# Kernel tuning notes

Hardware: AMD Instinct MI355X
Metric: run time of the kernel (lower is better)

The kernel has to match this reference:

```python
import jax, jax.numpy as jnp
import numpy as np

POOL_H, POOL_W = 7, 7


def _crop_and_resize(fmap, boxes, box_idx, ph, pw):
    """TF tf.image.crop_and_resize (bilinear) for normalized boxes.
    fmap: [B,H,W,C], boxes: [M,4] (y1,x1,y2,x2), box_idx: [M] int32 -> [M,ph,pw,C]."""
    H, W = fmap.shape[1], fmap.shape[2]
    dt = fmap.dtype
    y1, x1, y2, x2 = jnp.split(boxes.astype(dt), 4, axis=1)  # each [M,1]
    gy = jnp.arange(ph, dtype=dt) / (ph - 1)
    gx = jnp.arange(pw, dtype=dt) / (pw - 1)
    ys = (y1 + (y2 - y1) * gy[None, :]) * (H - 1)  # [M,ph]
    xs = (x1 + (x2 - x1) * gx[None, :]) * (W - 1)  # [M,pw]
    y0 = jnp.clip(jnp.floor(ys), 0, H - 1).astype(jnp.int32)
    x0 = jnp.clip(jnp.floor(xs), 0, W - 1).astype(jnp.int32)
    y1i = jnp.minimum(y0 + 1, H - 1)
    x1i = jnp.minimum(x0 + 1, W - 1)
    ly = (ys - y0.astype(dt))[:, :, None, None]  # [M,ph,1,1]
    lx = (xs - x0.astype(dt))[:, None, :, None]  # [M,1,pw,1]
    b = box_idx[:, None, None]
    tl = fmap[b, y0[:, :, None], x0[:, None, :]]   # [M,ph,pw,C]
    tr = fmap[b, y0[:, :, None], x1i[:, None, :]]
    bl = fmap[b, y1i[:, :, None], x0[:, None, :]]
    br = fmap[b, y1i[:, :, None], x1i[:, None, :]]
    top = tl + (tr - tl) * lx
    bot = bl + (br - bl) * lx
    return top + (bot - top) * ly


def pyramid_roi_align(boxes, image_meta, feature_maps):
    B, N, _ = boxes.shape
    y1, x1, y2, x2 = jnp.split(boxes, 4, axis=2)
    h = y2 - y1
    w = x2 - x1
    image_shape = image_meta[0, 4:7]
    image_area = image_shape[0] * image_shape[1]
    roi_level = jnp.log2(jnp.sqrt(h * w) / (224.0 / jnp.sqrt(image_area)))
    roi_level = jnp.clip(4 + jnp.round(roi_level).astype(jnp.int32), 2, 5)
    roi_level = roi_level.reshape(B * N)  # squeeze axis 2 + flatten

    flat_boxes = boxes.reshape(B * N, 4)
    box_idx = jnp.repeat(jnp.arange(B, dtype=jnp.int32), N)
    C = feature_maps[0].shape[-1]
    pooled = jnp.zeros((B * N, POOL_H, POOL_W, C), dtype=feature_maps[0].dtype)
    # Equivalent to TF's gather/crop/sort-restore: each box pooled from its level.
    for i, level in enumerate(range(2, 6)):
        crop = _crop_and_resize(feature_maps[i], flat_boxes, box_idx, POOL_H, POOL_W)
        mask = (roi_level == level)[:, None, None, None]
        pooled = jnp.where(mask, crop, pooled)
    return pooled.reshape(B, N, POOL_H, POOL_W, C)


def setup_inputs() -> dict:
    key = jax.random.key(0)
    k1, k2, k3, k4, k5, k6, k7, k8 = jax.random.split(key, 8)
    B, N, C = 2, 1000, 256
    # boxes: normalized y1,x1,y2,x2 with sizes spanning all FPN levels
    sz = jax.random.uniform(k1, (B, N, 1), minval=0.02, maxval=0.8)
    yx1 = jax.random.uniform(k2, (B, N, 2)) * (1.0 - sz)
    boxes = jnp.concatenate([yx1[..., :1], yx1[..., 1:], yx1[..., :1] + sz, yx1[..., 1:] + sz], axis=2)
    # image_meta: image_shape (1024,1024,3) at indices 4:7
    meta = np.zeros((B, 93), dtype=np.float32)
    meta[:, 1:4] = [1024, 1024, 3]
    meta[:, 4:7] = [1024, 1024, 3]
    meta[:, 11] = 1.0
    return {
        "boxes": boxes.astype(jnp.float32),
        "image_meta": jnp.asarray(meta),
        "feat_p2": jax.random.normal(k3, (B, 256, 256, C), dtype=jnp.float32),
        "feat_p3": jax.random.normal(k4, (B, 128, 128, C), dtype=jnp.float32),
        "feat_p4": jax.random.normal(k5, (B, 64, 64, C), dtype=jnp.float32),
        "feat_p5": jax.random.normal(k6, (B, 32, 32, C), dtype=jnp.float32),
    }


def reference(boxes, image_meta, feat_p2, feat_p3, feat_p4, feat_p5):
    return pyramid_roi_align(boxes, image_meta, (feat_p2, feat_p3, feat_p4, feat_p5))
```

## Files before the change

### kernel.cpp

```cpp
#include <hip/hip_runtime.h>
#include <math.h>


#define POOLN 7
#define CCH 256

typedef float f32x4 __attribute__((ext_vector_type(4)));

struct __align__(16) PixRec {
    int   tl, tr, bl, br;
    float lx, ly;
    int   li, pad;
};

__global__ __launch_bounds__(256) void roi_prep_kernel(
    const float* __restrict__ boxes,
    const float* __restrict__ meta,
    PixRec* __restrict__ recs,
    int n_boxes, int boxes_per_batch)
{
    int t = blockIdx.x * blockDim.x + threadIdx.x;
    int total = n_boxes * 49;
    if (t >= total) return;

    int box = t / 49;
    int p   = t - box * 49;
    int py  = (p * 37) >> 8;
    int px  = p - py * 7;

    float by1 = boxes[4 * box + 0];
    float bx1 = boxes[4 * box + 1];
    float by2 = boxes[4 * box + 2];
    float bx2 = boxes[4 * box + 3];
    float h = by2 - by1, w = bx2 - bx1;

    float area  = meta[4] * meta[5];
    float scale = 224.0f / sqrtf(area);
    float rl    = log2f(sqrtf(h * w) / scale);
    int lvl = 4 + (int)rintf(rl);
    lvl = lvl < 2 ? 2 : (lvl > 5 ? 5 : lvl);
    int li = lvl - 2;
    int H  = 256 >> li;
    float hm1 = (float)(H - 1);
    int b = box / boxes_per_batch;

    float gy  = (float)py / 6.0f;
    float ys  = (by1 + h * gy) * hm1;
    float fy0 = fminf(fmaxf(floorf(ys), 0.0f), hm1);
    int y0  = (int)fy0;
    int y1i = min(y0 + 1, H - 1);

    float gx  = (float)px / 6.0f;
    float xs  = (bx1 + w * gx) * hm1;
    float fx0 = fminf(fmaxf(floorf(xs), 0.0f), hm1);
    int x0  = (int)fx0;
    int x1i = min(x0 + 1, H - 1);

    int row0 = (b * H + y0)  * H;
    int row1 = (b * H + y1i) * H;

    PixRec r;
    r.tl = (row0 + x0)  * CCH;
    r.tr = (row0 + x1i) * CCH;
    r.bl = (row1 + x0)  * CCH;
    r.br = (row1 + x1i) * CCH;
    r.lx = xs - fx0;
    r.ly = ys - fy0;
    r.li = li;
    r.pad = 0;
    recs[t] = r;
}

__device__ __forceinline__ f32x4 bilerp4(f32x4 tl, f32x4 tr, f32x4 bl, f32x4 br,
                                         float lx, float ly)
{
    f32x4 r;
    float top, bot;
    top = tl.x + (tr.x - tl.x) * lx; bot = bl.x + (br.x - bl.x) * lx; r.x = top + (bot - top) * ly;
    top = tl.y + (tr.y - tl.y) * lx; bot = bl.y + (br.y - bl.y) * lx; r.y = top + (bot - top) * ly;
    top = tl.z + (tr.z - tl.z) * lx; bot = bl.z + (br.z - bl.z) * lx; r.z = top + (bot - top) * ly;
    top = tl.w + (tr.w - tl.w) * lx; bot = bl.w + (br.w - bl.w) * lx; r.w = top + (bot - top) * ly;
    return r;
}

__global__ __launch_bounds__(256) void roi_gather_kernel(
    const PixRec* __restrict__ recs,
    const float* __restrict__ f2,
    const float* __restrict__ f3,
    const float* __restrict__ f4,
    const float* __restrict__ f5,
    float* __restrict__ out,
    int q, int r, long total)
{
    int bid    = blockIdx.x;
    int xcd    = bid & 7;
    int within = bid >> 3;
    int wg = (xcd < r ? xcd * (q + 1) : r * (q + 1) + (xcd - r) * q) + within;

    long wid = (long)wg * 256 + threadIdx.x;
    if (wid >= total) return;

    int  c4  = (int)(wid & 31);
    long t   = wid >> 5;

    PixRec rec = recs[t];
    const float* f = (rec.li == 0) ? f2 : (rec.li == 1) ? f3 : (rec.li == 2) ? f4 : f5;
    float lx = rec.lx, ly = rec.ly;

    int co = c4 * 4;
    const float* ptl = f + rec.tl + co;
    const float* ptr2= f + rec.tr + co;
    const float* pbl = f + rec.bl + co;
    const float* pbr = f + rec.br + co;

    f32x4 tlA = *(const f32x4*)ptl;
    f32x4 trA = *(const f32x4*)ptr2;
    f32x4 blA = *(const f32x4*)pbl;
    f32x4 brA = *(const f32x4*)pbr;
    f32x4 tlB = *(const f32x4*)(ptl + 128);
    f32x4 trB = *(const f32x4*)(ptr2 + 128);
    f32x4 blB = *(const f32x4*)(pbl + 128);
    f32x4 brB = *(const f32x4*)(pbr + 128);

    f32x4 rA = bilerp4(tlA, trA, blA, brA, lx, ly);
    f32x4 rB = bilerp4(tlB, trB, blB, brB, lx, ly);

    long obase = t * CCH + co;
    __builtin_nontemporal_store(rA, (f32x4*)(out + obase));
    __builtin_nontemporal_store(rB, (f32x4*)(out + obase + 128));
}

__global__ __launch_bounds__(256) void roi_align_kernel(
    const float* __restrict__ boxes,
    const float* __restrict__ meta,
    const float* __restrict__ f2,
    const float* __restrict__ f3,
    const float* __restrict__ f4,
    const float* __restrict__ f5,
    float* __restrict__ out,
    int boxes_per_batch,
    long total4)
{
    long idx = (long)blockIdx.x * blockDim.x + threadIdx.x;
    if (idx >= total4) return;

    int c4  = (int)(idx & 63);
    long t  = idx >> 6;
    int p   = (int)(t % 49);
    int box = (int)(t / 49);
    int py = p / 7, px = p % 7;

    float by1 = boxes[4 * box + 0];
    float bx1 = boxes[4 * box + 1];
    float by2 = boxes[4 * box + 2];
    float bx2 = boxes[4 * box + 3];

    float h = by2 - by1, w = bx2 - bx1;
    float area  = meta[4] * meta[5];
    float scale = 224.0f / sqrtf(area);
    float rl    = log2f(sqrtf(h * w) / scale);
    int lvl = 4 + (int)rintf(rl);
    lvl = lvl < 2 ? 2 : (lvl > 5 ? 5 : lvl);
    int li = lvl - 2;
    const float* f = (li == 0) ? f2 : (li == 1) ? f3 : (li == 2) ? f4 : f5;
    int H = 256 >> li;

    int b = box / boxes_per_batch;

    float gy = (float)py / 6.0f;
    float gx = (float)px / 6.0f;
    float ys = (by1 + (by2 - by1) * gy) * (float)(H - 1);
    float xs = (bx1 + (bx2 - bx1) * gx) * (float)(H - 1);

    float fy0 = fminf(fmaxf(floorf(ys), 0.0f), (float)(H - 1));
    float fx0 = fminf(fmaxf(floorf(xs), 0.0f), (float)(H - 1));
    int y0 = (int)fy0, x0 = (int)fx0;
    int y1i = min(y0 + 1, H - 1);
    int x1i = min(x0 + 1, H - 1);
    float ly = ys - fy0;
    float lx = xs - fx0;

    size_t row0 = ((size_t)b * H + y0)  * H;
    size_t row1 = ((size_t)b * H + y1i) * H;
    const f32x4* tl = (const f32x4*)(f + (row0 + x0)  * CCH) + c4;
    const f32x4* tr = (const f32x4*)(f + (row0 + x1i) * CCH) + c4;
    const f32x4* bl = (const f32x4*)(f + (row1 + x0)  * CCH) + c4;
    const f32x4* br = (const f32x4*)(f + (row1 + x1i) * CCH) + c4;

    f32x4 rr = bilerp4(*tl, *tr, *bl, *br, lx, ly);
    ((f32x4*)out)[idx] = rr;
}

extern "C" void kernel_launch(void* const* d_in, const int* in_sizes, int n_in,
                              void* d_out, int out_size, void* d_ws, size_t ws_size,
                              hipStream_t stream) {
    const float* boxes = (const float*)d_in[0];
    const float* meta  = (const float*)d_in[1];
    const float* f2    = (const float*)d_in[2];
    const float* f3    = (const float*)d_in[3];
    const float* f4    = (const float*)d_in[4];
    const float* f5    = (const float*)d_in[5];
    float* out         = (float*)d_out;

    int n_boxes = in_sizes[0] / 4;
    int B       = in_sizes[2] / (256 * 256 * 256);
    int boxes_per_batch = n_boxes / B;

    int    n_pix = n_boxes * 49;
    size_t need  = (size_t)n_pix * sizeof(PixRec);

    if (d_ws != nullptr && ws_size >= need) {
        PixRec* recs = (PixRec*)d_ws;

        roi_prep_kernel<<<(n_pix + 255) / 256, 256, 0, stream>>>(
            boxes, meta, recs, n_boxes, boxes_per_batch);

        long total = (long)n_pix * 32;
        int  nwg   = (int)((total + 255) / 256);
        int  q = nwg >> 3, r = nwg & 7;
        roi_gather_kernel<<<nwg, 256, 0, stream>>>(
            recs, f2, f3, f4, f5, out, q, r, total);
    } else {
        long total4 = (long)n_boxes * 49 * 64;
        int  blocks = (int)((total4 + 255) / 256);
        roi_align_kernel<<<blocks, 256, 0, stream>>>(
            boxes, meta, f2, f3, f4, f5, out, boxes_per_batch, total4);
    }
}
```

Before: 42.61 us.

## Process boxes grouped by pyramid level via counting-sort order in gather

Adds a single-block kernel that computes each box's FPN level and builds a level-sorted box order using a shared-memory counting sort. The gather kernel then visits boxes in that order, so consecutive workgroups read from the same feature map, which should improve cache locality. The XCD-aware block remapping is removed in the same change. The cost is an extra serial one-block launch and an indirection load per thread. Because atomic ranks are nondeterministic, the order within a level is not stable.

```diff
diff --git a/kernel.cpp b/kernel.cpp
--- a/kernel.cpp
+++ b/kernel.cpp
@@ -12,6 +12,45 @@
     float lx, ly;
     int   li, pad;
 };
+
+__global__ __launch_bounds__(1024) void roi_sort_kernel(
+    const float* __restrict__ boxes,
+    const float* __restrict__ meta,
+    int* __restrict__ order,
+    int* __restrict__ li_box,
+    int* __restrict__ rank_box,
+    int n_boxes)
+{
+    __shared__ int scnt[4];
+    __shared__ int sbase[4];
+    int tid = threadIdx.x;
+    if (tid < 4) scnt[tid] = 0;
+    __syncthreads();
+
+    float area  = meta[4] * meta[5];
+    float scale = 224.0f / sqrtf(area);
+
+    for (int b = tid; b < n_boxes; b += blockDim.x) {
+        float by1 = boxes[4*b+0], bx1 = boxes[4*b+1];
+        float by2 = boxes[4*b+2], bx2 = boxes[4*b+3];
+        float h = by2 - by1, w = bx2 - bx1;
+        float rl = log2f(sqrtf(h * w) / scale);
+        int lvl = 4 + (int)rintf(rl);
+        lvl = lvl < 2 ? 2 : (lvl > 5 ? 5 : lvl);
+        int li = lvl - 2;
+        li_box[b]   = li;
+        rank_box[b] = atomicAdd(&scnt[li], 1);
+    }
+    __syncthreads();
+    if (tid == 0) {
+        int acc = 0;
+        for (int i = 0; i < 4; ++i) { sbase[i] = acc; acc += scnt[i]; }
+    }
+    __syncthreads();
+    for (int b = tid; b < n_boxes; b += blockDim.x) {
+        order[sbase[li_box[b]] + rank_box[b]] = b;
+    }
+}
 
 __global__ __launch_bounds__(256) void roi_prep_kernel(
     const float* __restrict__ boxes,
@@ -84,26 +123,27 @@
 }
 
 __global__ __launch_bounds__(256) void roi_gather_kernel(
+    const int* __restrict__ order,
     const PixRec* __restrict__ recs,
     const float* __restrict__ f2,
     const float* __restrict__ f3,
     const float* __restrict__ f4,
     const float* __restrict__ f5,
     float* __restrict__ out,
-    int q, int r, long total)
-{
-    int bid    = blockIdx.x;
-    int xcd    = bid & 7;
-    int within = bid >> 3;
-    int wg = (xcd < r ? xcd * (q + 1) : r * (q + 1) + (xcd - r) * q) + within;
-
-    long wid = (long)wg * 256 + threadIdx.x;
+    long total)
+{
+    long wid = (long)blockIdx.x * 256 + threadIdx.x;
     if (wid >= total) return;
 
-    int  c4  = (int)(wid & 31);
-    long t   = wid >> 5;
-
-    PixRec rec = recs[t];
+    int  c4   = (int)(wid & 31);
+    long t    = wid >> 5;
+    int  sbox = (int)(t / 49);
+    int  p    = (int)(t - (long)sbox * 49);
+
+    int box = order[sbox];
+    long bp = (long)box * 49 + p;
+
+    PixRec rec = recs[bp];
     const float* f = (rec.li == 0) ? f2 : (rec.li == 1) ? f3 : (rec.li == 2) ? f4 : f5;
     float lx = rec.lx, ly = rec.ly;
 
@@ -125,7 +165,7 @@
     f32x4 rA = bilerp4(tlA, trA, blA, brA, lx, ly);
     f32x4 rB = bilerp4(tlB, trB, blB, brB, lx, ly);
 
-    long obase = t * CCH + co;
+    long obase = bp * CCH + co;
     __builtin_nontemporal_store(rA, (f32x4*)(out + obase));
     __builtin_nontemporal_store(rB, (f32x4*)(out + obase + 128));
 }
@@ -206,20 +246,27 @@
     int B       = in_sizes[2] / (256 * 256 * 256);
     int boxes_per_batch = n_boxes / B;
 
-    int    n_pix = n_boxes * 49;
-    size_t need  = (size_t)n_pix * sizeof(PixRec);
+    int    n_pix     = n_boxes * 49;
+    size_t rec_bytes = (size_t)n_pix * sizeof(PixRec);
+    size_t int_bytes = (size_t)n_boxes * sizeof(int);
+    size_t need      = rec_bytes + 3 * int_bytes + 256;
 
     if (d_ws != nullptr && ws_size >= need) {
-        PixRec* recs = (PixRec*)d_ws;
+        PixRec* recs     = (PixRec*)d_ws;
+        int*    order    = (int*)((char*)d_ws + rec_bytes);
+        int*    li_box   = order + n_boxes;
+        int*    rank_box = li_box + n_boxes;
+
+        roi_sort_kernel<<<1, 1024, 0, stream>>>(
+            boxes, meta, order, li_box, rank_box, n_boxes);
 
         roi_prep_kernel<<<(n_pix + 255) / 256, 256, 0, stream>>>(
             boxes, meta, recs, n_boxes, boxes_per_batch);
 
         long total = (long)n_pix * 32;
         int  nwg   = (int)((total + 255) / 256);
-        int  q = nwg >> 3, r = nwg & 7;
         roi_gather_kernel<<<nwg, 256, 0, stream>>>(
-            recs, f2, f3, f4, f5, out, q, r, total);
+            order, recs, f2, f3, f4, f5, out, total);
     } else {
         long total4 = (long)n_boxes * 49 * 64;
         int  blocks = (int)((total4 + 255) / 256);
```

Result: slower. 48.19 us (+13.1%).
